# Optimization experiments

Hardware: AMD Instinct MI355X
Metric: run time of the kernel (lower is better)

## Reference

```python
import jax, jax.numpy as jnp
import numpy as np

B, N, D, H, NC = 4, 32, 128, 8, 27
DK = D // H
DFF = 4 * D
L = NC * N


def layer_norm(x, g, b, eps=1e-5):
    mu = jnp.mean(x, -1, keepdims=True)
    var = jnp.var(x, -1, keepdims=True)
    return (x - mu) * jax.lax.rsqrt(var + eps) * g + b


def setup_inputs() -> dict:
    ks = jax.random.split(jax.random.key(0), 16)
    s = 1.0 / np.sqrt(D)
    return {
        'x': jax.random.normal(ks[0], (B, N, D), jnp.float32),
        'mask': jax.random.randint(ks[1], (B, 1, N), 0, 2, jnp.int32),
        'coords': jax.random.normal(ks[2], (B, NC, N, 3), jnp.float32),
        'Wp': jax.random.normal(ks[3], (3, D), jnp.float32) * 0.5,
        'bp': jnp.zeros((D,), jnp.float32),
        'Wq': jax.random.normal(ks[4], (D, D), jnp.float32) * s,
        'bq': jnp.zeros((D,), jnp.float32),
        'Wk': jax.random.normal(ks[5], (D, D), jnp.float32) * s,
        'bk': jnp.zeros((D,), jnp.float32),
        'Wv': jax.random.normal(ks[6], (D, D), jnp.float32) * s,
        'bv': jnp.zeros((D,), jnp.float32),
        'Wo': jax.random.normal(ks[7], (D, D), jnp.float32) * s,
        'bo': jnp.zeros((D,), jnp.float32),
        'g1': jnp.ones((D,), jnp.float32),
        'b1': jnp.zeros((D,), jnp.float32),
        'g2': jnp.ones((D,), jnp.float32),
        'b2': jnp.zeros((D,), jnp.float32),
        'W1': jax.random.normal(ks[8], (D, DFF), jnp.float32) * s,
        'bf1': jnp.zeros((DFF,), jnp.float32),
        'W2': jax.random.normal(ks[9], (DFF, D), jnp.float32) * (1.0 / np.sqrt(DFF)),
        'bf2': jnp.zeros((D,), jnp.float32),
    }


def reference(x, mask, coords, Wp, bp, Wq, bq, Wk, bk, Wv, bv, Wo, bo,
              g1, b1, g2, b2, W1, bf1, W2, bf2):
    mask_enh = jnp.tile(mask, (1, NC, 1)).reshape(B, 1, 1, L)

    def step(i):
        # position_encoding: x broadcast over 27 images + linear of coords relative to atom i
        ci = jax.lax.dynamic_slice_in_dim(coords, i, 1, axis=2)        # [B,NC,1,3]
        ar = x[:, None] + (coords - ci) @ Wp + bp                      # [B,NC,N,D]
        a = ar.reshape(B, L, D)
        hn = layer_norm(a, g1, b1)
        q = (hn @ Wq + bq).reshape(B, L, H, DK).transpose(0, 2, 1, 3)
        k = (hn @ Wk + bk).reshape(B, L, H, DK).transpose(0, 2, 1, 3)
        v = (hn @ Wv + bv).reshape(B, L, H, DK).transpose(0, 2, 1, 3)
        scores = jnp.einsum('bhqd,bhkd->bhqk', q, k) / np.sqrt(DK)     # [B,H,L,L]
        scores = jnp.where(mask_enh == 0, -1e9, scores)
        att = jnp.einsum('bhqk,bhkd->bhqd', jax.nn.softmax(scores, -1), v)
        att = att.transpose(0, 2, 1, 3).reshape(B, L, D) @ Wo + bo
        s = a + att  # SublayerConnection (dropout identity in eval)
        # original keeps only [b, image 0, atom i] of the [B,NC,N,D] reshape; flat index = i
        return jax.lax.dynamic_slice_in_dim(s, i, 1, axis=1)[:, 0]     # [B,D]

    rows = jax.lax.map(step, jnp.arange(N))                            # [N,B,D]
    y = rows.transpose(1, 0, 2)                                        # [B,N,D]
    hn2 = layer_norm(y, g2, b2)
    return y + (jax.nn.relu(hn2 @ W1 + bf1) @ W2 + bf2)
```

## Files before the change

kernel.cpp:

```cpp
#include <hip/hip_runtime.h>


#define B_ 4
#define N_ 32
#define D_ 128
#define H_ 8
#define NC_ 27
#define DFF_ 512
#define L_ (NC_*N_)

__device__ __forceinline__ float wred(float v){
  #pragma unroll
  for (int off = 32; off; off >>= 1) v += __shfl_xor(v, off);
  return v;
}

__global__ __launch_bounds__(1024) void k_fused(
    const float* __restrict__ x, const int* __restrict__ mask,
    const float* __restrict__ coords,
    const float* __restrict__ Wp, const float* __restrict__ bp,
    const float* __restrict__ Wq, const float* __restrict__ bq,
    const float* __restrict__ Wk, const float* __restrict__ bk,
    const float* __restrict__ Wv, const float* __restrict__ bv,
    const float* __restrict__ Wo, const float* __restrict__ bo,
    const float* __restrict__ g1, const float* __restrict__ b1,
    const float* __restrict__ g2, const float* __restrict__ b2,
    const float* __restrict__ W1, const float* __restrict__ bf1,
    const float* __restrict__ W2, const float* __restrict__ bfb2,
    float* __restrict__ out)
{
  __shared__ float is_s[L_];
  __shared__ float dc_s[3][L_];
  __shared__ float xg_s[N_][D_+1];
  __shared__ float zz_s[H_][D_+1];
  __shared__ float w_s[3][D_];
  __shared__ float wcg_s[3][D_];
  __shared__ float g1_s[D_], b1_s[D_], bp_s[D_], bq_s[D_], bk_s[D_];
  __shared__ float g2_s[D_], b2_s[D_], bv_s[D_], bo_s[D_], bfb2_s[D_];
  __shared__ float bf1_s[DFF_];
  __shared__ float q_s[D_], hn_s[D_], hn2_s[D_], att_s[D_], y_s[D_];
  __shared__ float qAxk_s[H_][N_];
  __shared__ float qGk_s[H_][3];
  __shared__ float S3_s[H_];
  __shared__ float varx_s[N_];
  __shared__ float dxp_s[N_][3];
  __shared__ int   mask_s[N_];
  __shared__ float cq_s[NC_][3];
  __shared__ float mwp_s[3], P6_s[6];
  __shared__ float pmax_s[H_][2];
  __shared__ float Tnp_s[H_][2][N_];
  __shared__ float Sp_s[H_][2], RDp_s[H_][2][3];
  __shared__ float f_s[DFF_];
  __shared__ float pf_s[4096];
  float4* pf4 = (float4*)pf_s;

  int bi = blockIdx.x;
  int b = bi >> 5, i = bi & 31;
  int tid = threadIdx.x, wave = tid >> 6, lane = tid & 63;
  int es = tid >> 5, d4 = tid & 31;
  int e0 = 2*lane, e1 = 2*lane+1;

  int r0 = wave*2, r1 = wave*2+1;
  float2 xA = *(const float2*)&x[(size_t)(b*N_+r0)*D_ + e0];
  float2 xB = *(const float2*)&x[(size_t)(b*N_+r1)*D_ + e0];
  float2 xI = {0.f, 0.f};
  if (wave == 0) xI = *(const float2*)&x[(size_t)bi*D_ + e0];
  float ck0=0.f, ck1=0.f, ck2=0.f;
  if (tid < L_){
    int c = tid >> 5, n = tid & 31;
    const float* ck = coords + ((size_t)(b*NC_+c)*N_ + n)*3;
    ck0 = ck[0]; ck1 = ck[1]; ck2 = ck[2];
  }
  float4 wq4[4];
  #pragma unroll
  for (int k=0;k<4;k++)
    wq4[k] = *(const float4*)(Wq + (size_t)(es*4+k)*D_ + d4*4);
  float4 wk4[4];
  {
    int h = tid>>7, e = tid&127;
    #pragma unroll
    for (int k=0;k<4;k++)
      wk4[k] = *(const float4*)(Wk + (size_t)e*D_ + h*16 + k*4);
  }
  if (tid < 384) w_s[tid>>7][tid&127] = Wp[tid];
  if      (tid < 128)  g1_s[tid]      = g1[tid];
  else if (tid < 256)  b1_s[tid-128]  = b1[tid-128];
  else if (tid < 384)  bp_s[tid-256]  = bp[tid-256];
  else if (tid < 512)  bq_s[tid-384]  = bq[tid-384];
  else if (tid < 640)  bk_s[tid-512]  = bk[tid-512];
  else if (tid < 768)  g2_s[tid-640]  = g2[tid-640];
  else if (tid < 896)  b2_s[tid-768]  = b2[tid-768];
  else                 bv_s[tid-896]  = bv[tid-896];
  if      (tid < 128)  bo_s[tid]      = bo[tid];
  else if (tid < 256)  bfb2_s[tid-128]= bfb2[tid-128];
  else if (tid < 768)  bf1_s[tid-256] = bf1[tid-256];
  else if (tid < 800)  mask_s[tid-768]= mask[b*N_ + (tid-768)];
  else if (tid < 881){
    int t = tid-800;
    cq_s[t/3][t%3] = coords[((size_t)(b*NC_ + t/3)*N_ + i)*3 + t%3];
  }
  __syncthreads();

  {
    float t0 = xA.x + bp_s[e0], t1 = xA.y + bp_s[e1];
    float mean = wred(t0+t1)*(1.f/D_);
    float h0 = t0-mean, h1 = t1-mean;
    xg_s[r0][e0] = h0*g1_s[e0];
    xg_s[r0][e1] = h1*g1_s[e1];
    float vv = h0*h0 + h1*h1;
    float d0 = h0*w_s[0][e0] + h1*w_s[0][e1];
    float d1 = h0*w_s[1][e0] + h1*w_s[1][e1];
    float d2 = h0*w_s[2][e0] + h1*w_s[2][e1];
    #pragma unroll
    for (int off=32; off; off>>=1){
      vv += __shfl_xor(vv,off); d0 += __shfl_xor(d0,off);
      d1 += __shfl_xor(d1,off); d2 += __shfl_xor(d2,off);
    }
    if (lane==0){ varx_s[r0]=vv*(1.f/D_);
      dxp_s[r0][0]=d0; dxp_s[r0][1]=d1; dxp_s[r0][2]=d2; }
    if (r0 == i){
      float isq = rsqrtf(vv*(1.f/D_)+1e-5f);
      hn_s[e0] = h0*isq*g1_s[e0] + b1_s[e0];
      hn_s[e1] = h1*isq*g1_s[e1] + b1_s[e1];
    }
    t0 = xB.x + bp_s[e0]; t1 = xB.y + bp_s[e1];
    mean = wred(t0+t1)*(1.f/D_);
    h0 = t0-mean; h1 = t1-mean;
    xg_s[r1][e0] = h0*g1_s[e0];
    xg_s[r1][e1] = h1*g1_s[e1];
    vv = h0*h0 + h1*h1;
    d0 = h0*w_s[0][e0] + h1*w_s[0][e1];
    d1 = h0*w_s[1][e0] + h1*w_s[1][e1];
    d2 = h0*w_s[2][e0] + h1*w_s[2][e1];
    #pragma unroll
    for (int off=32; off; off>>=1){
      vv += __shfl_xor(vv,off); d0 += __shfl_xor(d0,off);
      d1 += __shfl_xor(d1,off); d2 += __shfl_xor(d2,off);
    }
    if (lane==0){ varx_s[r1]=vv*(1.f/D_);
      dxp_s[r1][0]=d0; dxp_s[r1][1]=d1; dxp_s[r1][2]=d2; }
    if (r1 == i){
      float isq = rsqrtf(vv*(1.f/D_)+1e-5f);
      hn_s[e0] = h0*isq*g1_s[e0] + b1_s[e0];
      hn_s[e1] = h1*isq*g1_s[e1] + b1_s[e1];
    }
  }
  float dc0=0.f, dc1=0.f, dc2=0.f;
  if (tid < L_){
    int c = tid >> 5;
    dc0 = ck0 - cq_s[c][0]; dc1 = ck1 - cq_s[c][1]; dc2 = ck2 - cq_s[c][2];
    dc_s[0][tid]=dc0; dc_s[1][tid]=dc1; dc_s[2][tid]=dc2;
  }
  if (wave >= 8 && wave < 11){
    int j = wave - 8;
    float s = w_s[j][lane] + w_s[j][lane+64];
    s = wred(s);
    if (lane==0) mwp_s[j] = s*(1.f/D_);
  }
  if (wave >= 10){
    int idx = wave - 10;
    int ja = (idx>=3) + (idx>=5);
    int jb = idx - (idx>=3)*2 - (idx>=5);
    float s = w_s[ja][lane]*w_s[jb][lane] + w_s[ja][lane+64]*w_s[jb][lane+64];
    s = wred(s);
    if (lane==0) P6_s[idx] = s;
  }
  __syncthreads();

  {
    float4 acc = {0.f,0.f,0.f,0.f};
    #pragma unroll
    for (int k=0;k<4;k++){
      float h = hn_s[es*4+k];
      acc.x += h*wq4[k].x; acc.y += h*wq4[k].y;
      acc.z += h*wq4[k].z; acc.w += h*wq4[k].w;
    }
    pf4[es*32 + d4] = acc;
  }
  if (tid < L_){
    int n = tid & 31;
    float m0 = mwp_s[0], m1 = mwp_s[1], m2 = mwp_s[2];
    float M00 = P6_s[0]-D_*m0*m0, M01 = P6_s[1]-D_*m0*m1;
    float M02 = P6_s[2]-D_*m0*m2, M11 = P6_s[3]-D_*m1*m1;
    float M12 = P6_s[4]-D_*m1*m2, M22 = P6_s[5]-D_*m2*m2;
    float quad = dc0*dc0*M00 + dc1*dc1*M11 + dc2*dc2*M22
               + 2.f*(dc0*dc1*M01 + dc0*dc2*M02 + dc1*dc2*M12);
    float lin  = dc0*dxp_s[n][0] + dc1*dxp_s[n][1] + dc2*dxp_s[n][2];
    float E = varx_s[n] + (quad + 2.f*lin)*(1.f/D_);
    is_s[tid] = rsqrtf(fmaxf(E, 0.f) + 1e-5f);
  }
  if (tid < 384){ int j=tid>>7, e=tid&127;
    wcg_s[j][e] = (w_s[j][e] - mwp_s[j])*g1_s[e]; }
  __syncthreads();

  if (tid < D_){
    float a = bq_s[tid];
    #pragma unroll
    for (int s=0;s<32;s++) a += pf_s[s*D_+tid];
    q_s[tid] = a;
  }
  __syncthreads();

  {
    int h = tid>>7, e = tid&127;
    float s = 0.f;
    #pragma unroll
    for (int kq=0; kq<4; kq++){
      s += wk4[kq].x*q_s[h*16+kq*4+0] + wk4[kq].y*q_s[h*16+kq*4+1]
         + wk4[kq].z*q_s[h*16+kq*4+2] + wk4[kq].w*q_s[h*16+kq*4+3];
    }
    zz_s[h][e] = s;
  }
  __syncthreads();

  {
    int quarter = tid>>8, id = tid&255, h = id>>5, n = id&31;
    float s = 0.f;
    #pragma unroll 8
    for (int e = quarter*32; e < quarter*32+32; e++) s += xg_s[n][e]*zz_s[h][e];
    pf_s[quarter*256 + id] = s;
  }
  __syncthreads();

  if (tid < 256){
    qAxk_s[tid>>5][tid&31] = pf_s[tid] + pf_s[256+tid]
                           + pf_s[512+tid] + pf_s[768+tid];
  }
  if (wave >= 8){
    int h = wave - 8;
    float u0 = zz_s[h][lane], u1 = zz_s[h][lane+64];
    float s3 = b1_s[lane]*u0 + b1_s[lane+64]*u1;
    if (lane < 16) s3 += q_s[h*16+lane]*bk_s[h*16+lane];
    float qg0 = wcg_s[0][lane]*u0 + wcg_s[0][lane+64]*u1;
    float qg1 = wcg_s[1][lane]*u0 + wcg_s[1][lane+64]*u1;
    float qg2 = wcg_s[2][lane]*u0 + wcg_s[2][lane+64]*u1;
    #pragma unroll
    for (int off=32; off; off>>=1){
      s3  += __shfl_xor(s3,off);  qg0 += __shfl_xor(qg0,off);
      qg1 += __shfl_xor(qg1,off); qg2 += __shfl_xor(qg2,off);
    }
    if (lane==0){ S3_s[h]=s3; qGk_s[h][0]=qg0; qGk_s[h][1]=qg1; qGk_s[h][2]=qg2; }
  }
  __syncthreads();

  int h2 = wave>>1, sub = wave&1, n2 = lane&31, half2 = lane>>5;
  int q4 = sub*2 + half2, c0 = q4*7, c1 = (q4==3) ? NC_ : c0+7;
  float4 wv4[4];
  #pragma unroll
  for (int k=0;k<4;k++)
    wv4[k] = *(const float4*)(Wv + (size_t)(es*4+k)*D_ + d4*4);
  {
    float qa = qAxk_s[h2][n2];
    float qg0 = qGk_s[h2][0], qg1 = qGk_s[h2][1], qg2 = qGk_s[h2][2];
    float s3 = S3_s[h2];
    bool mk = mask_s[n2] != 0;
    float sc[7];
    float M = -3.0e38f;
    #pragma unroll
    for (int t=0; t<7; t++){
      int c = c0+t;
      if (c < c1){
        int l = c*N_ + n2;
        float v = 0.25f*(is_s[l]*(qa + dc_s[0][l]*qg0 + dc_s[1][l]*qg1
                                     + dc_s[2][l]*qg2) + s3);
        sc[t] = mk ? v : -1e9f;
      } else sc[t] = -3.0e38f;
      M = fmaxf(M, sc[t]);
    }
    #pragma unroll
    for (int off=32; off; off>>=1) M = fmaxf(M, __shfl_xor(M, off));
    if (lane==0) pmax_s[h2][sub] = M;
    float S=0.f, Tn=0.f, rr0=0.f, rr1=0.f, rr2=0.f;
    #pragma unroll
    for (int t=0; t<7; t++){
      int c = c0+t;
      if (c < c1){
        int l = c*N_ + n2;
        float w_ = __expf(sc[t] - M);
        float tt = w_ * is_s[l];
        S += w_; Tn += tt;
        rr0 += tt*dc_s[0][l]; rr1 += tt*dc_s[1][l]; rr2 += tt*dc_s[2][l];
      }
    }
    float Tn2 = Tn + __shfl_xor(Tn, 32);
    if (lane < 32) Tnp_s[h2][sub][lane] = Tn2;
    #pragma unroll
    for (int off=32; off; off>>=1){
      S   += __shfl_xor(S,off);   rr0 += __shfl_xor(rr0,off);
      rr1 += __shfl_xor(rr1,off); rr2 += __shfl_xor(rr2,off);
    }
    if (lane==0){ Sp_s[h2][sub]=S;
      RDp_s[h2][sub][0]=rr0; RDp_s[h2][sub][1]=rr1; RDp_s[h2][sub][2]=rr2; }
  }
  __syncthreads();

  float4 wo4[4];
  #pragma unroll
  for (int k=0;k<4;k++)
    wo4[k] = *(const float4*)(Wo + (size_t)(es*4+k)*D_ + d4*4);
  {
    int h = tid>>7, e = tid&127;
    float M0 = pmax_s[h][0], M1 = pmax_s[h][1];
    float Mx = fmaxf(M0, M1);
    float f0 = __expf(M0-Mx), f1 = __expf(M1-Mx);
    float S = Sp_s[h][0]*f0 + Sp_s[h][1]*f1;
    float rS = 1.f / fmaxf(S, 1e-30f);
    float z = 0.f;
    #pragma unroll 8
    for (int n=0; n<N_; n++){
      float Tn = Tnp_s[h][0][n]*f0 + Tnp_s[h][1][n]*f1;
      z += Tn * xg_s[n][e];
    }
    float R0 = RDp_s[h][0][0]*f0 + RDp_s[h][1][0]*f1;
    float R1 = RDp_s[h][0][1]*f0 + RDp_s[h][1][1]*f1;
    float R2 = RDp_s[h][0][2]*f0 + RDp_s[h][1][2]*f1;
    z += R0*wcg_s[0][e] + R1*wcg_s[1][e] + R2*wcg_s[2][e];
    zz_s[h][e] = z*rS + b1_s[e];
  }
  __syncthreads();

  {
    int h = d4 >> 2;
    float4 acc = {0.f,0.f,0.f,0.f};
    #pragma unroll
    for (int k=0;k<4;k++){
      float zv = zz_s[h][es*4+k];
      acc.x += zv*wv4[k].x; acc.y += zv*wv4[k].y;
      acc.z += zv*wv4[k].z; acc.w += zv*wv4[k].w;
    }
    pf4[es*32 + d4] = acc;
  }
  __syncthreads();

  if (tid < D_){
    float a = bv_s[tid];
    #pragma unroll
    for (int s=0;s<32;s++) a += pf_s[s*D_+tid];
    att_s[tid] = a;
  }
  __syncthreads();

  int e8 = tid>>7, c4 = tid&127;
  float4 w14[16];
  #pragma unroll
  for (int k=0;k<16;k++)
    w14[k] = *(const float4*)(W1 + (size_t)(e8*16+k)*DFF_ + c4*4);
  {
    float4 acc = {0.f,0.f,0.f,0.f};
    #pragma unroll
    for (int k=0;k<4;k++){
      float av = att_s[es*4+k];
      acc.x += av*wo4[k].x; acc.y += av*wo4[k].y;
      acc.z += av*wo4[k].z; acc.w += av*wo4[k].w;
    }
    pf4[es*32 + d4] = acc;
  }
  __syncthreads();

  if (wave == 0){
    float y0 = xI.x + bp_s[e0] + bo_s[e0];
    float y1 = xI.y + bp_s[e1] + bo_s[e1];
    #pragma unroll
    for (int s=0;s<32;s++){
      float2 p = *(const float2*)&pf_s[s*D_ + e0];
      y0 += p.x; y1 += p.y;
    }
    y_s[e0] = y0; y_s[e1] = y1;
    float mean = wred(y0+y1)*(1.f/D_);
    float v0 = y0-mean, v1 = y1-mean;
    float var = wred(v0*v0+v1*v1)*(1.f/D_);
    float isd = rsqrtf(var + 1e-5f);
    hn2_s[e0] = v0*isd*g2_s[e0] + b2_s[e0];
    hn2_s[e1] = v1*isd*g2_s[e1] + b2_s[e1];
  }
  __syncthreads();

  {
    float4 acc = {0.f,0.f,0.f,0.f};
    #pragma unroll
    for (int k=0;k<16;k++){
      float h = hn2_s[e8*16+k];
      acc.x += h*w14[k].x; acc.y += h*w14[k].y;
      acc.z += h*w14[k].z; acc.w += h*w14[k].w;
    }
    pf4[e8*128 + c4] = acc;
  }
  __syncthreads();

  int js = tid>>5;
  float4 w24[16];
  #pragma unroll
  for (int k=0;k<16;k++)
    w24[k] = *(const float4*)(W2 + (size_t)(js*16+k)*D_ + d4*4);
  if (tid < DFF_){
    float a = bf1_s[tid];
    #pragma unroll
    for (int s=0;s<8;s++) a += pf_s[s*DFF_+tid];
    f_s[tid] = fmaxf(a, 0.f);
  }
  __syncthreads();

  {
    float4 acc = {0.f,0.f,0.f,0.f};
    #pragma unroll
    for (int k=0;k<16;k++){
      float fv = f_s[js*16+k];
      acc.x += fv*w24[k].x; acc.y += fv*w24[k].y;
      acc.z += fv*w24[k].z; acc.w += fv*w24[k].w;
    }
    pf4[js*32 + d4] = acc;
  }
  __syncthreads();

  if (tid < D_){
    float a = y_s[tid] + bfb2_s[tid];
    #pragma unroll
    for (int s=0;s<32;s++) a += pf_s[s*D_+tid];
    out[(size_t)bi*D_ + tid] = a;
  }
}

extern "C" void kernel_launch(void* const* d_in, const int* in_sizes, int n_in,
                              void* d_out, int out_size, void* d_ws, size_t ws_size,
                              hipStream_t stream){
  const float* x      = (const float*)d_in[0];
  const int*   mask   = (const int*)  d_in[1];
  const float* coords = (const float*)d_in[2];
  const float* Wp     = (const float*)d_in[3];
  const float* bp     = (const float*)d_in[4];
  const float* Wq     = (const float*)d_in[5];
  const float* bq     = (const float*)d_in[6];
  const float* Wk     = (const float*)d_in[7];
  const float* bk     = (const float*)d_in[8];
  const float* Wv     = (const float*)d_in[9];
  const float* bv     = (const float*)d_in[10];
  const float* Wo     = (const float*)d_in[11];
  const float* bo     = (const float*)d_in[12];
  const float* g1     = (const float*)d_in[13];
  const float* b1     = (const float*)d_in[14];
  const float* g2     = (const float*)d_in[15];
  const float* b2     = (const float*)d_in[16];
  const float* W1     = (const float*)d_in[17];
  const float* bf1    = (const float*)d_in[18];
  const float* W2     = (const float*)d_in[19];
  const float* bfb2   = (const float*)d_in[20];

  k_fused<<<B_*N_, 1024, 0, stream>>>(x, mask, coords, Wp, bp, Wq, bq, Wk, bk,
                                      Wv, bv, Wo, bo, g1, b1, g2, b2,
                                      W1, bf1, W2, bfb2, (float*)d_out);
}
```

Baseline: 115.4 us.

## Replace shared-memory partial-sum reductions with wave shuffle reductions in matvecs

```diff
diff --git a/kernel.cpp b/kernel.cpp
--- a/kernel.cpp
+++ b/kernel.cpp
@@ -38,10 +38,7 @@
   __shared__ float g1_s[D_], b1_s[D_], bp_s[D_], bq_s[D_], bk_s[D_];
   __shared__ float g2_s[D_], b2_s[D_], bv_s[D_], bo_s[D_], bfb2_s[D_];
   __shared__ float bf1_s[DFF_];
-  __shared__ float q_s[D_], hn_s[D_], hn2_s[D_], att_s[D_], y_s[D_];
-  __shared__ float qAxk_s[H_][N_];
-  __shared__ float qGk_s[H_][3];
-  __shared__ float S3_s[H_];
+  __shared__ float q_s[D_], hn_s[D_], hn2_s[D_], att_s[D_], y_s[D_], xi_s[D_];
   __shared__ float varx_s[N_];
   __shared__ float dxp_s[N_][3];
   __shared__ int   mask_s[N_];
@@ -51,30 +48,26 @@
   __shared__ float Tnp_s[H_][2][N_];
   __shared__ float Sp_s[H_][2], RDp_s[H_][2][3];
   __shared__ float f_s[DFF_];
-  __shared__ float pf_s[4096];
-  float4* pf4 = (float4*)pf_s;
 
   int bi = blockIdx.x;
   int b = bi >> 5, i = bi & 31;
   int tid = threadIdx.x, wave = tid >> 6, lane = tid & 63;
-  int es = tid >> 5, d4 = tid & 31;
+  int eg = lane >> 3, dl = lane & 7;
+  int dq = 8*wave + dl;
   int e0 = 2*lane, e1 = 2*lane+1;
 
   int r0 = wave*2, r1 = wave*2+1;
   float2 xA = *(const float2*)&x[(size_t)(b*N_+r0)*D_ + e0];
   float2 xB = *(const float2*)&x[(size_t)(b*N_+r1)*D_ + e0];
-  float2 xI = {0.f, 0.f};
-  if (wave == 0) xI = *(const float2*)&x[(size_t)bi*D_ + e0];
   float ck0=0.f, ck1=0.f, ck2=0.f;
   if (tid < L_){
     int c = tid >> 5, n = tid & 31;
     const float* ck = coords + ((size_t)(b*NC_+c)*N_ + n)*3;
     ck0 = ck[0]; ck1 = ck[1]; ck2 = ck[2];
   }
-  float4 wq4[4];
-  #pragma unroll
-  for (int k=0;k<4;k++)
-    wq4[k] = *(const float4*)(Wq + (size_t)(es*4+k)*D_ + d4*4);
+  float wqr[16];
+  #pragma unroll
+  for (int k=0;k<16;k++) wqr[k] = Wq[(size_t)(8*k+eg)*D_ + dq];
   float4 wk4[4];
   {
     int h = tid>>7, e = tid&127;
@@ -122,6 +115,7 @@
       float isq = rsqrtf(vv*(1.f/D_)+1e-5f);
       hn_s[e0] = h0*isq*g1_s[e0] + b1_s[e0];
       hn_s[e1] = h1*isq*g1_s[e1] + b1_s[e1];
+      xi_s[e0] = t0; xi_s[e1] = t1;
     }
     t0 = xB.x + bp_s[e0]; t1 = xB.y + bp_s[e1];
     mean = wred(t0+t1)*(1.f/D_);
@@ -143,6 +137,7 @@
       float isq = rsqrtf(vv*(1.f/D_)+1e-5f);
       hn_s[e0] = h0*isq*g1_s[e0] + b1_s[e0];
       hn_s[e1] = h1*isq*g1_s[e1] + b1_s[e1];
+      xi_s[e0] = t0; xi_s[e1] = t1;
     }
   }
   float dc0=0.f, dc1=0.f, dc2=0.f;
@@ -168,14 +163,11 @@
   __syncthreads();
 
   {
-    float4 acc = {0.f,0.f,0.f,0.f};
-    #pragma unroll
-    for (int k=0;k<4;k++){
-      float h = hn_s[es*4+k];
-      acc.x += h*wq4[k].x; acc.y += h*wq4[k].y;
-      acc.z += h*wq4[k].z; acc.w += h*wq4[k].w;
-    }
-    pf4[es*32 + d4] = acc;
+    float acc = 0.f;
+    #pragma unroll
+    for (int k=0;k<16;k++) acc += wqr[k]*hn_s[8*k+eg];
+    acc += __shfl_xor(acc,8); acc += __shfl_xor(acc,16); acc += __shfl_xor(acc,32);
+    if (eg==0) q_s[dq] = acc + bq_s[dq];
   }
   if (tid < L_){
     int n = tid & 31;
@@ -193,14 +185,9 @@
     wcg_s[j][e] = (w_s[j][e] - mwp_s[j])*g1_s[e]; }
   __syncthreads();
 
-  if (tid < D_){
-    float a = bq_s[tid];
-    #pragma unroll
-    for (int s=0;s<32;s++) a += pf_s[s*D_+tid];
-    q_s[tid] = a;
-  }
-  __syncthreads();
-
+  float wvr[16];
+  #pragma unroll
+  for (int k=0;k<16;k++) wvr[k] = Wv[(size_t)(8*k+eg)*D_ + dq];
   {
     int h = tid>>7, e = tid&127;
     float s = 0.f;
@@ -213,24 +200,16 @@
   }
   __syncthreads();
 
-  {
-    int quarter = tid>>8, id = tid&255, h = id>>5, n = id&31;
-    float s = 0.f;
-    #pragma unroll 8
-    for (int e = quarter*32; e < quarter*32+32; e++) s += xg_s[n][e]*zz_s[h][e];
-    pf_s[quarter*256 + id] = s;
-  }
-  __syncthreads();
-
-  if (tid < 256){
-    qAxk_s[tid>>5][tid&31] = pf_s[tid] + pf_s[256+tid]
-                           + pf_s[512+tid] + pf_s[768+tid];
-  }
-  if (wave >= 8){
-    int h = wave - 8;
-    float u0 = zz_s[h][lane], u1 = zz_s[h][lane+64];
+  int h4 = wave>>1, sub = wave&1, n2 = lane&31, half2 = lane>>5;
+  int q4c = sub*2 + half2, c0 = q4c*7, c1 = (q4c==3) ? NC_ : c0+7;
+  {
+    float qa = 0.f;
+    #pragma unroll
+    for (int k=0;k<64;k++) qa += xg_s[n2][2*k+half2]*zz_s[h4][2*k+half2];
+    qa += __shfl_xor(qa, 32);
+    float u0 = zz_s[h4][lane], u1 = zz_s[h4][lane+64];
     float s3 = b1_s[lane]*u0 + b1_s[lane+64]*u1;
-    if (lane < 16) s3 += q_s[h*16+lane]*bk_s[h*16+lane];
+    if (lane < 16) s3 += q_s[h4*16+lane]*bk_s[h4*16+lane];
     float qg0 = wcg_s[0][lane]*u0 + wcg_s[0][lane+64]*u1;
     float qg1 = wcg_s[1][lane]*u0 + wcg_s[1][lane+64]*u1;
     float qg2 = wcg_s[2][lane]*u0 + wcg_s[2][lane+64]*u1;
@@ -239,20 +218,6 @@
       s3  += __shfl_xor(s3,off);  qg0 += __shfl_xor(qg0,off);
       qg1 += __shfl_xor(qg1,off); qg2 += __shfl_xor(qg2,off);
     }
-    if (lane==0){ S3_s[h]=s3; qGk_s[h][0]=qg0; qGk_s[h][1]=qg1; qGk_s[h][2]=qg2; }
-  }
-  __syncthreads();
-
-  int h2 = wave>>1, sub = wave&1, n2 = lane&31, half2 = lane>>5;
-  int q4 = sub*2 + half2, c0 = q4*7, c1 = (q4==3) ? NC_ : c0+7;
-  float4 wv4[4];
-  #pragma unroll
-  for (int k=0;k<4;k++)
-    wv4[k] = *(const float4*)(Wv + (size_t)(es*4+k)*D_ + d4*4);
-  {
-    float qa = qAxk_s[h2][n2];
-    float qg0 = qGk_s[h2][0], qg1 = qGk_s[h2][1], qg2 = qGk_s[h2][2];
-    float s3 = S3_s[h2];
     bool mk = mask_s[n2] != 0;
     float sc[7];
     float M = -3.0e38f;
@@ -269,7 +234,7 @@
     }
     #pragma unroll
     for (int off=32; off; off>>=1) M = fmaxf(M, __shfl_xor(M, off));
-    if (lane==0) pmax_s[h2][sub] = M;
+    if (lane==0) pmax_s[h4][sub] = M;
     float S=0.f, Tn=0.f, rr0=0.f, rr1=0.f, rr2=0.f;
     #pragma unroll
     for (int t=0; t<7; t++){
@@ -283,21 +248,20 @@
       }
     }
     float Tn2 = Tn + __shfl_xor(Tn, 32);
-    if (lane < 32) Tnp_s[h2][sub][lane] = Tn2;
+    if (lane < 32) Tnp_s[h4][sub][lane] = Tn2;
     #pragma unroll
     for (int off=32; off; off>>=1){
       S   += __shfl_xor(S,off);   rr0 += __shfl_xor(rr0,off);
       rr1 += __shfl_xor(rr1,off); rr2 += __shfl_xor(rr2,off);
     }
-    if (lane==0){ Sp_s[h2][sub]=S;
-      RDp_s[h2][sub][0]=rr0; RDp_s[h2][sub][1]=rr1; RDp_s[h2][sub][2]=rr2; }
-  }
-  __syncthreads();
-
-  float4 wo4[4];
-  #pragma unroll
-  for (int k=0;k<4;k++)
-    wo4[k] = *(const float4*)(Wo + (size_t)(es*4+k)*D_ + d4*4);
+    if (lane==0){ Sp_s[h4][sub]=S;
+      RDp_s[h4][sub][0]=rr0; RDp_s[h4][sub][1]=rr1; RDp_s[h4][sub][2]=rr2; }
+  }
+  __syncthreads();
+
+  float wor[16];
+  #pragma unroll
+  for (int k=0;k<16;k++) wor[k] = Wo[(size_t)(8*k+eg)*D_ + dq];
   {
     int h = tid>>7, e = tid&127;
     float M0 = pmax_s[h][0], M1 = pmax_s[h][1];
@@ -320,52 +284,30 @@
   __syncthreads();
 
   {
-    int h = d4 >> 2;
-    float4 acc = {0.f,0.f,0.f,0.f};
-    #pragma unroll
-    for (int k=0;k<4;k++){
-      float zv = zz_s[h][es*4+k];
-      acc.x += zv*wv4[k].x; acc.y += zv*wv4[k].y;
-      acc.z += zv*wv4[k].z; acc.w += zv*wv4[k].w;
-    }
-    pf4[es*32 + d4] = acc;
-  }
-  __syncthreads();
-
-  if (tid < D_){
-    float a = bv_s[tid];
-    #pragma unroll
-    for (int s=0;s<32;s++) a += pf_s[s*D_+tid];
-    att_s[tid] = a;
-  }
-  __syncthreads();
-
-  int e8 = tid>>7, c4 = tid&127;
-  float4 w14[16];
-  #pragma unroll
-  for (int k=0;k<16;k++)
-    w14[k] = *(const float4*)(W1 + (size_t)(e8*16+k)*DFF_ + c4*4);
-  {
-    float4 acc = {0.f,0.f,0.f,0.f};
-    #pragma unroll
-    for (int k=0;k<4;k++){
-      float av = att_s[es*4+k];
-      acc.x += av*wo4[k].x; acc.y += av*wo4[k].y;
-      acc.z += av*wo4[k].z; acc.w += av*wo4[k].w;
-    }
-    pf4[es*32 + d4] = acc;
-  }
-  __syncthreads();
-
+    int ha = wave>>1;
+    float acc = 0.f;
+    #pragma unroll
+    for (int k=0;k<16;k++) acc += wvr[k]*zz_s[ha][8*k+eg];
+    acc += __shfl_xor(acc,8); acc += __shfl_xor(acc,16); acc += __shfl_xor(acc,32);
+    if (eg==0) att_s[dq] = acc + bv_s[dq];
+  }
+  __syncthreads();
+
+  {
+    float acc = 0.f;
+    #pragma unroll
+    for (int k=0;k<16;k++) acc += wor[k]*att_s[8*k+eg];
+    acc += __shfl_xor(acc,8); acc += __shfl_xor(acc,16); acc += __shfl_xor(acc,32);
+    if (eg==0) y_s[dq] = xi_s[dq] + bo_s[dq] + acc;
+  }
+  __syncthreads();
+
+  int cl = lane & 31, eh = lane >> 5, col = 32*wave + cl;
+  float w1r[64];
+  #pragma unroll
+  for (int k=0;k<64;k++) w1r[k] = W1[(size_t)(2*k+eh)*DFF_ + col];
   if (wave == 0){
-    float y0 = xI.x + bp_s[e0] + bo_s[e0];
-    float y1 = xI.y + bp_s[e1] + bo_s[e1];
-    #pragma unroll
-    for (int s=0;s<32;s++){
-      float2 p = *(const float2*)&pf_s[s*D_ + e0];
-      y0 += p.x; y1 += p.y;
-    }
-    y_s[e0] = y0; y_s[e1] = y1;
+    float y0 = y_s[e0], y1 = y_s[e1];
     float mean = wred(y0+y1)*(1.f/D_);
     float v0 = y0-mean, v1 = y1-mean;
     float var = wred(v0*v0+v1*v1)*(1.f/D_);
@@ -375,48 +317,25 @@
   }
   __syncthreads();
 
-  {
-    float4 acc = {0.f,0.f,0.f,0.f};
-    #pragma unroll
-    for (int k=0;k<16;k++){
-      float h = hn2_s[e8*16+k];
-      acc.x += h*w14[k].x; acc.y += h*w14[k].y;
-      acc.z += h*w14[k].z; acc.w += h*w14[k].w;
-    }
-    pf4[e8*128 + c4] = acc;
-  }
-  __syncthreads();
-
-  int js = tid>>5;
-  float4 w24[16];
-  #pragma unroll
-  for (int k=0;k<16;k++)
-    w24[k] = *(const float4*)(W2 + (size_t)(js*16+k)*D_ + d4*4);
-  if (tid < DFF_){
-    float a = bf1_s[tid];
-    #pragma unroll
-    for (int s=0;s<8;s++) a += pf_s[s*DFF_+tid];
-    f_s[tid] = fmaxf(a, 0.f);
-  }
-  __syncthreads();
-
-  {
-    float4 acc = {0.f,0.f,0.f,0.f};
-    #pragma unroll
-    for (int k=0;k<16;k++){
-      float fv = f_s[js*16+k];
-      acc.x += fv*w24[k].x; acc.y += fv*w24[k].y;
-      acc.z += fv*w24[k].z; acc.w += fv*w24[k].w;
-    }
-    pf4[js*32 + d4] = acc;
-  }
-  __syncthreads();
-
-  if (tid < D_){
-    float a = y_s[tid] + bfb2_s[tid];
-    #pragma unroll
-    for (int s=0;s<32;s++) a += pf_s[s*D_+tid];
-    out[(size_t)bi*D_ + tid] = a;
+  int jg = lane >> 3;
+  float w2r[64];
+  {
+    float acc = 0.f;
+    #pragma unroll
+    for (int k=0;k<64;k++) acc += w1r[k]*hn2_s[2*k+eh];
+    acc += __shfl_xor(acc, 32);
+    if (eh==0) f_s[col] = fmaxf(acc + bf1_s[col], 0.f);
+  }
+  #pragma unroll
+  for (int k=0;k<64;k++) w2r[k] = W2[(size_t)(8*k+jg)*D_ + dq];
+  __syncthreads();
+
+  {
+    float acc = 0.f;
+    #pragma unroll
+    for (int k=0;k<64;k++) acc += w2r[k]*f_s[8*k+jg];
+    acc += __shfl_xor(acc,8); acc += __shfl_xor(acc,16); acc += __shfl_xor(acc,32);
+    if (jg==0) out[(size_t)bi*D_ + dq] = y_s[dq] + bfb2_s[dq] + acc;
   }
 }
 
```

Measured after the change: 120.2 us. 4.2% more time.
